# Kernel tuning notes

Measured on AMD Instinct MI355X. Metric: run time of the kernel, lower is better.

The kernel has to match this reference:

```python
import jax, jax.numpy as jnp
import numpy as np

B, N, F_IN, OUT = 1, 8192, 256, 64

def setup_inputs() -> dict:
    key = jax.random.key(0)
    k1, k2, k3, k4 = jax.random.split(key, 4)
    seq = jax.random.normal(k1, (B, N, F_IN), dtype=jnp.float32)
    bias_mat = jnp.zeros((B, N, N), dtype=jnp.float32)  # 0 = fully connected; -1e9 entries mask edges
    W1 = jax.random.normal(k2, (F_IN, OUT), dtype=jnp.float32) * 0.05
    a1 = jax.random.normal(k3, (OUT, 1), dtype=jnp.float32) * 0.05
    b1 = jnp.zeros((1,), dtype=jnp.float32)
    a2 = jax.random.normal(k4, (OUT, 1), dtype=jnp.float32) * 0.05
    b2 = jnp.zeros((1,), dtype=jnp.float32)
    return {"seq": seq, "bias_mat": bias_mat, "W1": W1, "a1": a1, "b1": b1, "a2": a2, "b2": b2}

def reference(seq, bias_mat, W1, a1, b1, a2, b2):
    # Conv1D(kernel=1) == matmul over the feature dim
    seq_fts = jnp.einsum('bnf,fo->bno', seq, W1)          # [B,N,OUT]
    f_1 = jnp.einsum('bno,ok->bnk', seq_fts, a1) + b1      # [B,N,1]
    f_2 = jnp.einsum('bno,ok->bnk', seq_fts, a2) + b2      # [B,N,1]
    logits = f_1 + jnp.swapaxes(f_2, 1, 2)                  # [B,N,N] additive outer-sum
    coefs = jax.nn.softmax(jax.nn.leaky_relu(logits, negative_slope=0.2) + bias_mat, axis=-1)
    vals = jnp.einsum('bnm,bmo->bno', coefs, seq_fts)       # [B,N,OUT]
    return jax.nn.elu(vals)
```

## Files before the change

kernel.cpp:

```cpp
#include <hip/hip_runtime.h>
#include <hip/hip_bf16.h>


typedef float f32x4 __attribute__((ext_vector_type(4)));
typedef short bf16x8 __attribute__((ext_vector_type(8)));

__device__ __forceinline__ unsigned short f2bf(float x) {
    union { float f; unsigned u; } v; v.f = x;
    unsigned r = v.u + 0x7FFF + ((v.u >> 16) & 1);
    return (unsigned short)(r >> 16);
}

__device__ __forceinline__ float elu1(float x) {
    return x > 0.f ? x : (__expf(x) - 1.f);
}

__global__ __launch_bounds__(256) void attn_fts(
    const float* __restrict__ seq, const float* __restrict__ W1,
    const float* __restrict__ a1, const float* __restrict__ b1,
    const float* __restrict__ a2, const float* __restrict__ b2,
    unsigned short* __restrict__ ftsT, float* __restrict__ f1g,
    float* __restrict__ f2g)
{
    __shared__ unsigned short w1t[64 * 264];
    __shared__ unsigned short stage[64 * 40];
    __shared__ float f1p[2][32];
    __shared__ float f2p[2][32];

    const int tid = threadIdx.x;
    const int qb = blockIdx.x * 32;
    const int w = tid >> 6, rg = w & 1, oh = w >> 1;
    const int lane = tid & 63, c = lane & 15, g = lane >> 4;

    for (int i = 0; i < 64; ++i) {
        int e = tid + i * 256;
        int k = e >> 6, o = e & 63;
        w1t[o * 264 + k] = f2bf(W1[e]);
    }
    __syncthreads();

    f32x4 acc[2] = {};
    const float* srow = seq + (long)(qb + rg * 16 + c) * 256;
    #pragma unroll
    for (int ks = 0; ks < 8; ++ks) {
        int k0 = ks * 32 + g * 8;
        float4 s0 = *(const float4*)(srow + k0);
        float4 s1 = *(const float4*)(srow + k0 + 4);
        bf16x8 af;
        af[0] = (short)f2bf(s0.x); af[1] = (short)f2bf(s0.y);
        af[2] = (short)f2bf(s0.z); af[3] = (short)f2bf(s0.w);
        af[4] = (short)f2bf(s1.x); af[5] = (short)f2bf(s1.y);
        af[6] = (short)f2bf(s1.z); af[7] = (short)f2bf(s1.w);
        #pragma unroll
        for (int ob = 0; ob < 2; ++ob) {
            int brow = oh * 32 + ob * 16 + c;
            bf16x8 bf = *(const bf16x8*)(&w1t[brow * 264 + k0]);
            acc[ob] = __builtin_amdgcn_mfma_f32_16x16x32_bf16(af, bf, acc[ob], 0, 0, 0);
        }
    }

    float a1v0 = a1[oh * 32 + c], a1v1 = a1[oh * 32 + 16 + c];
    float a2v0 = a2[oh * 32 + c], a2v1 = a2[oh * 32 + 16 + c];
    #pragma unroll
    for (int reg = 0; reg < 4; ++reg) {
        float p1 = acc[0][reg] * a1v0 + acc[1][reg] * a1v1;
        float p2 = acc[0][reg] * a2v0 + acc[1][reg] * a2v1;
        #pragma unroll
        for (int mm = 1; mm < 16; mm <<= 1) {
            p1 += __shfl_xor(p1, mm, 64);
            p2 += __shfl_xor(p2, mm, 64);
        }
        if (c == 0) {
            f1p[oh][rg * 16 + g * 4 + reg] = p1;
            f2p[oh][rg * 16 + g * 4 + reg] = p2;
        }
    }

    #pragma unroll
    for (int ob = 0; ob < 2; ++ob) {
        int row = oh * 32 + ob * 16 + c;
        #pragma unroll
        for (int rp = 0; rp < 2; ++rp) {
            unsigned short lo = f2bf(acc[ob][rp * 2]);
            unsigned short hi = f2bf(acc[ob][rp * 2 + 1]);
            unsigned v = (unsigned)lo | ((unsigned)hi << 16);
            *(unsigned*)(&stage[row * 40 + rg * 16 + g * 4 + rp * 2]) = v;
        }
    }
    __syncthreads();

    {
        int o = tid >> 2, q4 = tid & 3;
        uint4 v = *(const uint4*)(&stage[o * 40 + q4 * 8]);
        *(uint4*)(&ftsT[(long)o * 8192 + qb + q4 * 8]) = v;
    }
    if (tid < 32) {
        f1g[qb + tid] = f1p[0][tid] + f1p[1][tid] + b1[0];
        f2g[qb + tid] = f2p[0][tid] + f2p[1][tid] + b2[0];
    }
}

__global__ __launch_bounds__(512, 4) void attn_main(
    const float* __restrict__ bias, const unsigned short* __restrict__ ftsT,
    const float* __restrict__ f1g, const float* __restrict__ f2g,
    float* __restrict__ out)
{
    __shared__ float macc[8][16][68];
    __shared__ float mlm[8][16];
    __shared__ float mll[8][16];

    const int tid = threadIdx.x;
    const int qb = blockIdx.x * 16;
    const int h = tid >> 6;
    const int lane = tid & 63, c = lane & 15, g = lane >> 4;

    const float f1r = f1g[qb + c];

    const float* bias_base = bias + (long)(qb + c) * 8192 + h * 32 + g * 8;
    const unsigned short* fts_base = ftsT + (long)c * 8192 + h * 32 + g * 8;
    const float* f2_base = f2g + h * 32 + g * 8;

    float4 bA0, bA1, bB0, bB1;
    bf16x8 fA0, fA1, fA2, fA3, fB0, fB1, fB2, fB3;
    float4 f2Aa, f2Ab, f2Ba, f2Bb;

    auto issueA = [&](int r) {
        const float* bp = bias_base + r * 256;
        bA0 = ((const float4*)bp)[0]; bA1 = ((const float4*)bp)[1];
        const unsigned short* fp = fts_base + r * 256;
        fA0 = *(const bf16x8*)(fp);
        fA1 = *(const bf16x8*)(fp + 16 * 8192);
        fA2 = *(const bf16x8*)(fp + 32 * 8192);
        fA3 = *(const bf16x8*)(fp + 48 * 8192);
        const float* qp = f2_base + r * 256;
        f2Aa = ((const float4*)qp)[0]; f2Ab = ((const float4*)qp)[1];
    };
    auto issueB = [&](int r) {
        const float* bp = bias_base + r * 256;
        bB0 = ((const float4*)bp)[0]; bB1 = ((const float4*)bp)[1];
        const unsigned short* fp = fts_base + r * 256;
        fB0 = *(const bf16x8*)(fp);
        fB1 = *(const bf16x8*)(fp + 16 * 8192);
        fB2 = *(const bf16x8*)(fp + 32 * 8192);
        fB3 = *(const bf16x8*)(fp + 48 * 8192);
        const float* qp = f2_base + r * 256;
        f2Ba = ((const float4*)qp)[0]; f2Bb = ((const float4*)qp)[1];
    };

    float m = -INFINITY, lsum = 0.f;
    f32x4 acc[4] = {};

    auto do_round = [&](const float4& b0, const float4& b1v,
                        const bf16x8& ff0, const bf16x8& ff1,
                        const bf16x8& ff2, const bf16x8& ff3,
                        const float4& fa, const float4& fb) {
        float bb[8] = { b0.x, b0.y, b0.z, b0.w, b1v.x, b1v.y, b1v.z, b1v.w };
        float f2v[8] = { fa.x, fa.y, fa.z, fa.w, fb.x, fb.y, fb.z, fb.w };
        float s[8];
        float tm = -INFINITY;
        #pragma unroll
        for (int i = 0; i < 8; ++i) {
            float z = f1r + f2v[i];
            z = fmaxf(z, 0.2f * z);
            float sv = z + bb[i];
            s[i] = sv;
            tm = fmaxf(tm, sv);
        }
        tm = fmaxf(tm, __shfl_xor(tm, 16, 64));
        tm = fmaxf(tm, __shfl_xor(tm, 32, 64));
        if (!__all(tm <= m + 8.f)) {
            float mnew = fmaxf(m, tm);
            float sc = __expf(m - mnew);
            lsum *= sc;
            float scq[4];
            #pragma unroll
            for (int reg = 0; reg < 4; ++reg) scq[reg] = __shfl(sc, g * 4 + reg, 64);
            #pragma unroll
            for (int ob = 0; ob < 4; ++ob)
                #pragma unroll
                for (int reg = 0; reg < 4; ++reg) acc[ob][reg] *= scq[reg];
            m = mnew;
        }
        float ts = 0.f;
        bf16x8 af;
        #pragma unroll
        for (int i = 0; i < 8; ++i) {
            float p = __expf(s[i] - m);
            ts += p;
            af[i] = (short)f2bf(p);
        }
        ts += __shfl_xor(ts, 16, 64);
        ts += __shfl_xor(ts, 32, 64);
        lsum += ts;
        acc[0] = __builtin_amdgcn_mfma_f32_16x16x32_bf16(af, ff0, acc[0], 0, 0, 0);
        acc[1] = __builtin_amdgcn_mfma_f32_16x16x32_bf16(af, ff1, acc[1], 0, 0, 0);
        acc[2] = __builtin_amdgcn_mfma_f32_16x16x32_bf16(af, ff2, acc[2], 0, 0, 0);
        acc[3] = __builtin_amdgcn_mfma_f32_16x16x32_bf16(af, ff3, acc[3], 0, 0, 0);
    };

    issueA(0);
    issueB(1);

    #pragma unroll 1
    for (int rp = 0; rp < 16; ++rp) {
        do_round(bA0, bA1, fA0, fA1, fA2, fA3, f2Aa, f2Ab);
        if (rp < 15) issueA(2 * rp + 2);
        do_round(bB0, bB1, fB0, fB1, fB2, fB3, f2Ba, f2Bb);
        if (rp < 15) issueB(2 * rp + 3);
    }

    #pragma unroll
    for (int ob = 0; ob < 4; ++ob)
        #pragma unroll
        for (int reg = 0; reg < 4; ++reg)
            macc[h][g * 4 + reg][ob * 16 + c] = acc[ob][reg];
    if (lane < 16) { mlm[h][c] = m; mll[h][c] = lsum; }
    __syncthreads();

    if (tid < 256) {
        const int row = tid >> 4;
        const int o0 = (tid & 15) * 4;
        float ms = -INFINITY;
        #pragma unroll
        for (int sI = 0; sI < 8; ++sI) ms = fmaxf(ms, mlm[sI][row]);
        float den = 0.f;
        float vx = 0.f, vy = 0.f, vz = 0.f, vw = 0.f;
        #pragma unroll
        for (int sI = 0; sI < 8; ++sI) {
            float ws = __expf(mlm[sI][row] - ms);
            den += mll[sI][row] * ws;
            float4 a = *(const float4*)(&macc[sI][row][o0]);
            vx += a.x * ws; vy += a.y * ws; vz += a.z * ws; vw += a.w * ws;
        }
        float inv = 1.f / den;
        float4 res;
        res.x = elu1(vx * inv); res.y = elu1(vy * inv);
        res.z = elu1(vz * inv); res.w = elu1(vw * inv);
        *(float4*)(&out[(long)(qb + row) * 64 + o0]) = res;
    }
}

extern "C" void kernel_launch(void* const* d_in, const int* in_sizes, int n_in,
                              void* d_out, int out_size, void* d_ws, size_t ws_size,
                              hipStream_t stream) {
    (void)in_sizes; (void)n_in; (void)out_size; (void)ws_size;
    const float* seq  = (const float*)d_in[0];
    const float* bias = (const float*)d_in[1];
    const float* W1   = (const float*)d_in[2];
    const float* a1   = (const float*)d_in[3];
    const float* b1   = (const float*)d_in[4];
    const float* a2   = (const float*)d_in[5];
    const float* b2   = (const float*)d_in[6];
    float* out = (float*)d_out;

    unsigned short* ftsT = (unsigned short*)d_ws;
    float* f1 = (float*)((char*)d_ws + 64 * 8192 * 2);
    float* f2 = (float*)((char*)d_ws + 64 * 8192 * 2 + 8192 * 4);

    hipLaunchKernelGGL(attn_fts, dim3(256), dim3(256), 0, stream,
                       seq, W1, a1, b1, a2, b2, ftsT, f1, f2);
    hipLaunchKernelGGL(attn_main, dim3(512), dim3(512), 0, stream,
                       bias, ftsT, f1, f2, out);
}
```

Before: 411.2 us.

## Stage bias tiles into LDS via async global_load_lds with 4-wave blocks

The main attention kernel now stages each 16x256 tile of the bias matrix into double-buffered shared memory using direct global-to-LDS loads, with full-row coalesced accesses. Previously each lane loaded small strided bias chunks into registers. Blocks shrink from 8 to 4 waves, and each wave handles 64 columns per round over two k-steps, so the cross-wave merge is smaller. The cost is a block-wide barrier every round, fts and f2 loads that are no longer software-prefetched into registers, and fewer waves per block.

```diff
diff --git a/kernel.cpp b/kernel.cpp
--- a/kernel.cpp
+++ b/kernel.cpp
@@ -13,6 +13,13 @@
 
 __device__ __forceinline__ float elu1(float x) {
     return x > 0.f ? x : (__expf(x) - 1.f);
+}
+
+__device__ __forceinline__ void gld_lds16(const void* g, void* l) {
+    __builtin_amdgcn_global_load_lds(
+        (const __attribute__((address_space(1))) void*)(unsigned long long)g,
+        (__attribute__((address_space(3))) void*)(unsigned)(unsigned long long)l,
+        16, 0, 0);
 }
 
 __global__ __launch_bounds__(256) void attn_fts(
@@ -100,14 +107,15 @@
     }
 }
 
-__global__ __launch_bounds__(512, 4) void attn_main(
+__global__ __launch_bounds__(256) void attn_main(
     const float* __restrict__ bias, const unsigned short* __restrict__ ftsT,
     const float* __restrict__ f1g, const float* __restrict__ f2g,
     float* __restrict__ out)
 {
-    __shared__ float macc[8][16][68];
-    __shared__ float mlm[8][16];
-    __shared__ float mll[8][16];
+    __shared__ float blds[2][16][260];
+    __shared__ float macc[4][16][68];
+    __shared__ float mlm[4][16];
+    __shared__ float mll[4][16];
 
     const int tid = threadIdx.x;
     const int qb = blockIdx.x * 16;
@@ -116,44 +124,33 @@
 
     const float f1r = f1g[qb + c];
 
-    const float* bias_base = bias + (long)(qb + c) * 8192 + h * 32 + g * 8;
-    const unsigned short* fts_base = ftsT + (long)c * 8192 + h * 32 + g * 8;
-    const float* f2_base = f2g + h * 32 + g * 8;
-
-    float4 bA0, bA1, bB0, bB1;
-    bf16x8 fA0, fA1, fA2, fA3, fB0, fB1, fB2, fB3;
-    float4 f2Aa, f2Ab, f2Ba, f2Bb;
-
-    auto issueA = [&](int r) {
-        const float* bp = bias_base + r * 256;
-        bA0 = ((const float4*)bp)[0]; bA1 = ((const float4*)bp)[1];
-        const unsigned short* fp = fts_base + r * 256;
-        fA0 = *(const bf16x8*)(fp);
-        fA1 = *(const bf16x8*)(fp + 16 * 8192);
-        fA2 = *(const bf16x8*)(fp + 32 * 8192);
-        fA3 = *(const bf16x8*)(fp + 48 * 8192);
-        const float* qp = f2_base + r * 256;
-        f2Aa = ((const float4*)qp)[0]; f2Ab = ((const float4*)qp)[1];
-    };
-    auto issueB = [&](int r) {
-        const float* bp = bias_base + r * 256;
-        bB0 = ((const float4*)bp)[0]; bB1 = ((const float4*)bp)[1];
-        const unsigned short* fp = fts_base + r * 256;
-        fB0 = *(const bf16x8*)(fp);
-        fB1 = *(const bf16x8*)(fp + 16 * 8192);
-        fB2 = *(const bf16x8*)(fp + 32 * 8192);
-        fB3 = *(const bf16x8*)(fp + 48 * 8192);
-        const float* qp = f2_base + r * 256;
-        f2Ba = ((const float4*)qp)[0]; f2Bb = ((const float4*)qp)[1];
-    };
-
     float m = -INFINITY, lsum = 0.f;
     f32x4 acc[4] = {};
 
-    auto do_round = [&](const float4& b0, const float4& b1v,
-                        const bf16x8& ff0, const bf16x8& ff1,
-                        const bf16x8& ff2, const bf16x8& ff3,
-                        const float4& fa, const float4& fb) {
+    auto issue_round = [&](int r, int buf) {
+        #pragma unroll
+        for (int i = 0; i < 4; ++i) {
+            const int row = h * 4 + i;
+            const float* gsrc = bias + (long)(qb + row) * 8192 + r * 256 + lane * 4;
+            gld_lds16(gsrc, &blds[buf][row][0]);
+        }
+    };
+
+    auto do_ks = [&](int r, int ks) {
+        const int jcol = h * 64 + ks * 32 + g * 8;
+        const float* bl = &blds[r & 1][c][jcol];
+        float4 b0 = *(const float4*)(bl);
+        float4 b1v = *(const float4*)(bl + 4);
+        const int jg = r * 256 + jcol;
+        const unsigned short* fp = ftsT + (long)c * 8192 + jg;
+        bf16x8 ff0 = *(const bf16x8*)(fp);
+        bf16x8 ff1 = *(const bf16x8*)(fp + 16 * 8192);
+        bf16x8 ff2 = *(const bf16x8*)(fp + 32 * 8192);
+        bf16x8 ff3 = *(const bf16x8*)(fp + 48 * 8192);
+        const float* qp = f2g + jg;
+        float4 fa = ((const float4*)qp)[0];
+        float4 fb = ((const float4*)qp)[1];
+
         float bb[8] = { b0.x, b0.y, b0.z, b0.w, b1v.x, b1v.y, b1v.z, b1v.w };
         float f2v[8] = { fa.x, fa.y, fa.z, fa.w, fb.x, fb.y, fb.z, fb.w };
         float s[8];
@@ -172,13 +169,15 @@
             float mnew = fmaxf(m, tm);
             float sc = __expf(m - mnew);
             lsum *= sc;
-            float scq[4];
+            float scq0 = __shfl(sc, g * 4 + 0, 64);
+            float scq1 = __shfl(sc, g * 4 + 1, 64);
+            float scq2 = __shfl(sc, g * 4 + 2, 64);
+            float scq3 = __shfl(sc, g * 4 + 3, 64);
             #pragma unroll
-            for (int reg = 0; reg < 4; ++reg) scq[reg] = __shfl(sc, g * 4 + reg, 64);
-            #pragma unroll
-            for (int ob = 0; ob < 4; ++ob)
-                #pragma unroll
-                for (int reg = 0; reg < 4; ++reg) acc[ob][reg] *= scq[reg];
+            for (int ob = 0; ob < 4; ++ob) {
+                acc[ob][0] *= scq0; acc[ob][1] *= scq1;
+                acc[ob][2] *= scq2; acc[ob][3] *= scq3;
+            }
             m = mnew;
         }
         float ts = 0.f;
@@ -198,44 +197,46 @@
         acc[3] = __builtin_amdgcn_mfma_f32_16x16x32_bf16(af, ff3, acc[3], 0, 0, 0);
     };
 
-    issueA(0);
-    issueB(1);
-
+    issue_round(0, 0);
     #pragma unroll 1
-    for (int rp = 0; rp < 16; ++rp) {
-        do_round(bA0, bA1, fA0, fA1, fA2, fA3, f2Aa, f2Ab);
-        if (rp < 15) issueA(2 * rp + 2);
-        do_round(bB0, bB1, fB0, fB1, fB2, fB3, f2Ba, f2Bb);
-        if (rp < 15) issueB(2 * rp + 3);
-    }
-
-    #pragma unroll
-    for (int ob = 0; ob < 4; ++ob)
-        #pragma unroll
-        for (int reg = 0; reg < 4; ++reg)
-            macc[h][g * 4 + reg][ob * 16 + c] = acc[ob][reg];
+    for (int r = 0; r < 32; ++r) {
+        __syncthreads();
+        if (r + 1 < 32) issue_round(r + 1, (r + 1) & 1);
+        do_ks(r, 0);
+        do_ks(r, 1);
+    }
+
+    __syncthreads();
+    #pragma unroll
+    for (int ob = 0; ob < 4; ++ob) {
+        macc[h][g * 4 + 0][ob * 16 + c] = acc[ob][0];
+        macc[h][g * 4 + 1][ob * 16 + c] = acc[ob][1];
+        macc[h][g * 4 + 2][ob * 16 + c] = acc[ob][2];
+        macc[h][g * 4 + 3][ob * 16 + c] = acc[ob][3];
+    }
     if (lane < 16) { mlm[h][c] = m; mll[h][c] = lsum; }
     __syncthreads();
 
-    if (tid < 256) {
+    {
         const int row = tid >> 4;
         const int o0 = (tid & 15) * 4;
-        float ms = -INFINITY;
-        #pragma unroll
-        for (int sI = 0; sI < 8; ++sI) ms = fmaxf(ms, mlm[sI][row]);
-        float den = 0.f;
-        float vx = 0.f, vy = 0.f, vz = 0.f, vw = 0.f;
-        #pragma unroll
-        for (int sI = 0; sI < 8; ++sI) {
-            float ws = __expf(mlm[sI][row] - ms);
-            den += mll[sI][row] * ws;
-            float4 a = *(const float4*)(&macc[sI][row][o0]);
-            vx += a.x * ws; vy += a.y * ws; vz += a.z * ws; vw += a.w * ws;
-        }
+        float m0 = mlm[0][row], m1 = mlm[1][row];
+        float m2 = mlm[2][row], m3 = mlm[3][row];
+        float ms = fmaxf(fmaxf(m0, m1), fmaxf(m2, m3));
+        float w0 = __expf(m0 - ms), w1 = __expf(m1 - ms);
+        float w2 = __expf(m2 - ms), w3 = __expf(m3 - ms);
+        float den = mll[0][row] * w0 + mll[1][row] * w1 +
+                    mll[2][row] * w2 + mll[3][row] * w3;
         float inv = 1.f / den;
+        float4 v0 = *(const float4*)(&macc[0][row][o0]);
+        float4 v1 = *(const float4*)(&macc[1][row][o0]);
+        float4 v2 = *(const float4*)(&macc[2][row][o0]);
+        float4 v3 = *(const float4*)(&macc[3][row][o0]);
         float4 res;
-        res.x = elu1(vx * inv); res.y = elu1(vy * inv);
-        res.z = elu1(vz * inv); res.w = elu1(vw * inv);
+        res.x = elu1((v0.x * w0 + v1.x * w1 + v2.x * w2 + v3.x * w3) * inv);
+        res.y = elu1((v0.y * w0 + v1.y * w1 + v2.y * w2 + v3.y * w3) * inv);
+        res.z = elu1((v0.z * w0 + v1.z * w1 + v2.z * w2 + v3.z * w3) * inv);
+        res.w = elu1((v0.w * w0 + v1.w * w1 + v2.w * w2 + v3.w * w3) * inv);
         *(float4*)(&out[(long)(qb + row) * 64 + o0]) = res;
     }
 }
@@ -259,6 +260,6 @@
 
     hipLaunchKernelGGL(attn_fts, dim3(256), dim3(256), 0, stream,
                        seq, W1, a1, b1, a2, b2, ftsT, f1, f2);
-    hipLaunchKernelGGL(attn_main, dim3(512), dim3(512), 0, stream,
+    hipLaunchKernelGGL(attn_main, dim3(512), dim3(256), 0, stream,
                        bias, ftsT, f1, f2, out);
 }
```

After: 395.8 us. 1.04x faster.
